# Optimization experiments

Measured on AMD Instinct MI355X. Metric: run time of the kernel, lower is better.

Reference implementation:

```python
import jax, jax.numpy as jnp
import numpy as np

N_USER, N_MOVIE, H, E = 100000, 50000, 512, 500000

def setup_inputs() -> dict:
    key = jax.random.key(0)
    ks = jax.random.split(key, 8)
    z_user = jax.random.normal(ks[0], (N_USER, H), dtype=jnp.float32)
    z_movie = jax.random.normal(ks[1], (N_MOVIE, H), dtype=jnp.float32)
    edge_row = jax.random.randint(ks[2], (E,), 0, N_USER, dtype=jnp.int64)
    edge_col = jax.random.randint(ks[3], (E,), 0, N_MOVIE, dtype=jnp.int64)
    w1 = jax.random.normal(ks[4], (2 * H, H), dtype=jnp.float32) * (1.0 / np.sqrt(2 * H))
    b1 = jax.random.normal(ks[5], (H,), dtype=jnp.float32) * 0.01
    w2 = jax.random.normal(ks[6], (H, 1), dtype=jnp.float32) * (1.0 / np.sqrt(H))
    b2 = jax.random.normal(ks[7], (1,), dtype=jnp.float32) * 0.01
    return {"z_user": z_user, "z_movie": z_movie, "edge_row": edge_row,
            "edge_col": edge_col, "w1": w1, "b1": b1, "w2": w2, "b2": b2}

def reference(z_user, z_movie, edge_row, edge_col, w1, b1, w2, b2):
    # Gather endpoint embeddings and concat -> [E, 2H]
    z = jnp.concatenate([z_user[edge_row], z_movie[edge_col]], axis=-1)
    h = jax.nn.relu(z @ w1 + b1)      # [E, H]
    out = h @ w2 + b2                 # [E, 1]
    return out.reshape(-1)
```

## Files before the change

kernel.cpp:

```cpp
#include <hip/hip_runtime.h>
#include <hip/hip_bf16.h>

typedef __attribute__((ext_vector_type(8))) short bf16x8;
typedef __attribute__((ext_vector_type(4))) float f32x4;

#define HDIM 512
#define BM 128
#define BN 256
#define BK 64
#define BKP 72

__device__ __forceinline__ unsigned short f2bf(float f) {
  unsigned u = __float_as_uint(f);
  u += 0x7fffu + ((u >> 16) & 1u);
  return (unsigned short)(u >> 16);
}

__device__ __forceinline__ unsigned int pk_bf(float x, float y) {
  __hip_bfloat162 h = __float22bfloat162_rn(float2{x, y});
  union { __hip_bfloat162 b; unsigned int u; } cv; cv.b = h;
  return cv.u;
}

__global__ void k_w1t(const float* __restrict__ w1, unsigned short* __restrict__ w1t,
                      int* __restrict__ cnt, int nzero) {
  int idx = blockIdx.x * 256 + threadIdx.x;
  int k = idx >> 9;
  int n = idx & 511;
  w1t[n * 1024 + k] = f2bf(w1[idx]);
  if (idx < nzero) cnt[idx] = 0;
}

__global__ void k_hist(const int* __restrict__ ec, int* __restrict__ cnt, int E) {
  int e = blockIdx.x * 256 + threadIdx.x;
  if (e < E) atomicAdd(&cnt[ec[e]], 1);
}

__global__ __launch_bounds__(1024) void k_scan(const int* __restrict__ cnt, int* __restrict__ ptr,
                                               int* __restrict__ cur, int n) {
  __shared__ int wsum[16];
  __shared__ int carry_s;
  const int tid = threadIdx.x, lane = tid & 63, w = tid >> 6;
  if (tid == 0) carry_s = 0;
  __syncthreads();
  for (int base = 0; base < n; base += 1024) {
    int i = base + tid;
    int x = (i < n) ? cnt[i] : 0;
    int v = x;
    #pragma unroll
    for (int off = 1; off < 64; off <<= 1) {
      int t = __shfl_up(v, off, 64);
      if (lane >= off) v += t;
    }
    if (lane == 63) wsum[w] = v;
    __syncthreads();
    int wpre = 0;
    #pragma unroll
    for (int j = 0; j < 16; ++j) { int s = wsum[j]; if (j < w) wpre += s; }
    int carry = carry_s;
    __syncthreads();
    int incl = v + wpre;
    if (i < n) { int excl = carry + incl - x; ptr[i] = excl; cur[i] = excl; }
    if (tid == 1023) carry_s = carry + incl;
    __syncthreads();
  }
  if (threadIdx.x == 0) ptr[n] = carry_s;
}

__global__ void k_scatter(const int* __restrict__ er, const int* __restrict__ ec,
                          int* __restrict__ cur, int* __restrict__ srow,
                          int* __restrict__ seid, int E) {
  int e = blockIdx.x * 256 + threadIdx.x;
  if (e < E) {
    int c = ec[e];
    int pos = atomicAdd(&cur[c], 1);
    srow[pos] = er[e];
    seid[pos] = e;
  }
}

__global__ __launch_bounds__(512) void k_gemm(const float* __restrict__ A, int M,
    const unsigned short* __restrict__ w1t, int koff,
    unsigned short* __restrict__ C)
{
  __shared__ unsigned short As[BM][BKP];
  __shared__ unsigned short Bs[BN][BKP];
  const int tid  = threadIdx.x;
  const int lane = tid & 63;
  const int wid  = tid >> 6;
  const int wm = wid & 1, wn = wid >> 1;
  const int lm = lane & 15, lq = lane >> 4;
  const int nbase = blockIdx.x * BN;
  const int mbase = blockIdx.y * BM;

  f32x4 acc[4][4];
  #pragma unroll
  for (int i = 0; i < 4; ++i)
    #pragma unroll
    for (int j = 0; j < 4; ++j) acc[i][j] = (f32x4){0.f, 0.f, 0.f, 0.f};

  for (int kb = 0; kb < HDIM / BK; ++kb) {
    const int k0 = kb * BK;
    __syncthreads();
    #pragma unroll
    for (int i = 0; i < 4; ++i) {
      int fid = i * 512 + tid;
      int r = fid >> 4, c4 = fid & 15;
      int row = mbase + r; if (row > M - 1) row = M - 1;
      const float4 v = *(const float4*)&A[(size_t)row * HDIM + k0 + c4 * 4];
      unsigned int* dst = (unsigned int*)&As[r][c4 * 4];
      dst[0] = pk_bf(v.x, v.y);
      dst[1] = pk_bf(v.z, v.w);
    }
    #pragma unroll
    for (int i = 0; i < 4; ++i) {
      int cid = i * 512 + tid;
      int r = cid >> 3, c8 = cid & 7;
      const bf16x8 g = *(const bf16x8*)&w1t[(size_t)(nbase + r) * 1024 + koff + k0 + c8 * 8];
      *(bf16x8*)&Bs[r][c8 * 8] = g;
    }
    __syncthreads();
    #pragma unroll
    for (int ks = 0; ks < 2; ++ks) {
      bf16x8 af[4], bfr[4];
      #pragma unroll
      for (int t = 0; t < 4; ++t) {
        af[t]  = *(const bf16x8*)&As[wm * 64 + t * 16 + lm][ks * 32 + lq * 8];
        bfr[t] = *(const bf16x8*)&Bs[wn * 64 + t * 16 + lm][ks * 32 + lq * 8];
      }
      #pragma unroll
      for (int mi = 0; mi < 4; ++mi)
        #pragma unroll
        for (int ni = 0; ni < 4; ++ni)
          acc[mi][ni] = __builtin_amdgcn_mfma_f32_16x16x32_bf16(af[mi], bfr[ni], acc[mi][ni], 0, 0, 0);
    }
  }
  #pragma unroll
  for (int mi = 0; mi < 4; ++mi)
    #pragma unroll
    for (int ni = 0; ni < 4; ++ni)
      #pragma unroll
      for (int r = 0; r < 4; ++r) {
        int rg = mbase + wm * 64 + mi * 16 + lq * 4 + r;
        int cg = nbase + wn * 64 + ni * 16 + lm;
        if (rg < M) C[(size_t)rg * HDIM + cg] = f2bf(acc[mi][ni][r]);
      }
}

__device__ __forceinline__ float edot(const uint4 ua, const float* vb, const float* wv) {
  float p = 0.f, s;
  s = __uint_as_float(ua.x << 16)         + vb[0]; s = fmaxf(s, 0.f); p += s * wv[0];
  s = __uint_as_float(ua.x & 0xffff0000u) + vb[1]; s = fmaxf(s, 0.f); p += s * wv[1];
  s = __uint_as_float(ua.y << 16)         + vb[2]; s = fmaxf(s, 0.f); p += s * wv[2];
  s = __uint_as_float(ua.y & 0xffff0000u) + vb[3]; s = fmaxf(s, 0.f); p += s * wv[3];
  s = __uint_as_float(ua.z << 16)         + vb[4]; s = fmaxf(s, 0.f); p += s * wv[4];
  s = __uint_as_float(ua.z & 0xffff0000u) + vb[5]; s = fmaxf(s, 0.f); p += s * wv[5];
  s = __uint_as_float(ua.w << 16)         + vb[6]; s = fmaxf(s, 0.f); p += s * wv[6];
  s = __uint_as_float(ua.w & 0xffff0000u) + vb[7]; s = fmaxf(s, 0.f); p += s * wv[7];
  return p;
}

__global__ __launch_bounds__(256) void k_edge_g(const int* __restrict__ ptr,
    const int* __restrict__ srow, const int* __restrict__ seid,
    const unsigned short* __restrict__ u1, const unsigned short* __restrict__ m1,
    const float* __restrict__ b1, const float* __restrict__ w2, const float* __restrict__ b2,
    float* __restrict__ out, int nmov)
{
  const int lane = threadIdx.x & 63;
  const int gw = blockIdx.x * 4 + (threadIdx.x >> 6);
  const int nw = gridDim.x * 4;
  const float4 b1a = *(const float4*)&b1[lane * 8];
  const float4 b1b = *(const float4*)&b1[lane * 8 + 4];
  const float4 w2a = *(const float4*)&w2[lane * 8];
  const float4 w2b = *(const float4*)&w2[lane * 8 + 4];
  float wv[8] = {w2a.x, w2a.y, w2a.z, w2a.w, w2b.x, w2b.y, w2b.z, w2b.w};
  const float bias2 = b2[0];
  for (int c = gw; c < nmov; c += nw) {
    const int beg = ptr[c], end = ptr[c + 1];
    if (beg == end) continue;
    const uint4 va = *(const uint4*)&m1[(size_t)c * HDIM + lane * 8];
    float vb[8];
    vb[0] = __uint_as_float(va.x << 16)         + b1a.x;
    vb[1] = __uint_as_float(va.x & 0xffff0000u) + b1a.y;
    vb[2] = __uint_as_float(va.y << 16)         + b1a.z;
    vb[3] = __uint_as_float(va.y & 0xffff0000u) + b1a.w;
    vb[4] = __uint_as_float(va.z << 16)         + b1b.x;
    vb[5] = __uint_as_float(va.z & 0xffff0000u) + b1b.y;
    vb[6] = __uint_as_float(va.w << 16)         + b1b.z;
    vb[7] = __uint_as_float(va.w & 0xffff0000u) + b1b.w;
    int i = beg;
    for (; i + 1 < end; i += 2) {
      const int r0 = srow[i], r1 = srow[i + 1];
      const int e0 = seid[i], e1 = seid[i + 1];
      const uint4 ua0 = *(const uint4*)&u1[(size_t)r0 * HDIM + lane * 8];
      const uint4 ua1 = *(const uint4*)&u1[(size_t)r1 * HDIM + lane * 8];
      float p0 = edot(ua0, vb, wv);
      float p1 = edot(ua1, vb, wv);
      #pragma unroll
      for (int off = 32; off > 0; off >>= 1) {
        p0 += __shfl_down(p0, off, 64);
        p1 += __shfl_down(p1, off, 64);
      }
      if (lane == 0) { out[e0] = p0 + bias2; out[e1] = p1 + bias2; }
    }
    if (i < end) {
      const int r0 = srow[i], e0 = seid[i];
      const uint4 ua0 = *(const uint4*)&u1[(size_t)r0 * HDIM + lane * 8];
      float p0 = edot(ua0, vb, wv);
      #pragma unroll
      for (int off = 32; off > 0; off >>= 1) p0 += __shfl_down(p0, off, 64);
      if (lane == 0) out[e0] = p0 + bias2;
    }
  }
}

__global__ __launch_bounds__(256) void k_edge(const int* __restrict__ er, const int* __restrict__ ec,
    const unsigned short* __restrict__ u1, const unsigned short* __restrict__ m1,
    const float* __restrict__ b1, const float* __restrict__ w2, const float* __restrict__ b2,
    float* __restrict__ out, int E)
{
  const int lane = threadIdx.x & 63;
  const int gwid = blockIdx.x * 4 + (threadIdx.x >> 6);
  const int nw   = gridDim.x * 4;
  const float4 b1a = *(const float4*)&b1[lane * 8];
  const float4 b1b = *(const float4*)&b1[lane * 8 + 4];
  const float4 w2a = *(const float4*)&w2[lane * 8];
  const float4 w2b = *(const float4*)&w2[lane * 8 + 4];
  float bv[8] = {b1a.x, b1a.y, b1a.z, b1a.w, b1b.x, b1b.y, b1b.z, b1b.w};
  float wv[8] = {w2a.x, w2a.y, w2a.z, w2a.w, w2b.x, w2b.y, w2b.z, w2b.w};
  const float bias2 = b2[0];
  for (int e = gwid; e < E; e += nw) {
    const int r = er[e], c = ec[e];
    const uint4 ua = *(const uint4*)&u1[(size_t)r * HDIM + lane * 8];
    const uint4 va = *(const uint4*)&m1[(size_t)c * HDIM + lane * 8];
    float vb[8];
    vb[0] = __uint_as_float(va.x << 16)         + bv[0];
    vb[1] = __uint_as_float(va.x & 0xffff0000u) + bv[1];
    vb[2] = __uint_as_float(va.y << 16)         + bv[2];
    vb[3] = __uint_as_float(va.y & 0xffff0000u) + bv[3];
    vb[4] = __uint_as_float(va.z << 16)         + bv[4];
    vb[5] = __uint_as_float(va.z & 0xffff0000u) + bv[5];
    vb[6] = __uint_as_float(va.w << 16)         + bv[6];
    vb[7] = __uint_as_float(va.w & 0xffff0000u) + bv[7];
    float p = edot(ua, vb, wv);
    #pragma unroll
    for (int off = 32; off > 0; off >>= 1) p += __shfl_down(p, off, 64);
    if (lane == 0) out[e] = p + bias2;
  }
}

__global__ __launch_bounds__(256) void k_fallback(const float* __restrict__ zu, const float* __restrict__ zm,
    const int* __restrict__ er, const int* __restrict__ ec, const float* __restrict__ w1,
    const float* __restrict__ b1, const float* __restrict__ w2, const float* __restrict__ b2,
    float* __restrict__ out, int E)
{
  __shared__ float Zs[64][33];
  __shared__ float Ws[32][65];
  __shared__ float outacc[64];
  __shared__ int ridx[64], cidx[64];
  const int tid = threadIdx.x;
  const int ebase = blockIdx.x * 64;
  if (tid < 64) {
    int e = ebase + tid; if (e > E - 1) e = E - 1;
    ridx[tid] = er[e]; cidx[tid] = ec[e];
    outacc[tid] = 0.f;
  }
  const int tx = tid & 15, ty = tid >> 4;
  for (int nt = 0; nt < 8; ++nt) {
    float acc[4][4] = {};
    for (int kc = 0; kc < 32; ++kc) {
      __syncthreads();
      #pragma unroll
      for (int i = 0; i < 8; ++i) {
        int id = i * 256 + tid;
        int rr = id >> 5, cc = id & 31;
        int k = kc * 32 + cc;
        Zs[rr][cc] = (k < 512) ? zu[(size_t)ridx[rr] * 512 + k]
                               : zm[(size_t)cidx[rr] * 512 + (k - 512)];
      }
      #pragma unroll
      for (int i = 0; i < 8; ++i) {
        int id = i * 256 + tid;
        int kk = id >> 6, nn = id & 63;
        Ws[kk][nn] = w1[(size_t)(kc * 32 + kk) * 512 + nt * 64 + nn];
      }
      __syncthreads();
      #pragma unroll
      for (int kk = 0; kk < 32; ++kk) {
        float a0 = Zs[ty*4+0][kk], a1 = Zs[ty*4+1][kk], a2 = Zs[ty*4+2][kk], a3 = Zs[ty*4+3][kk];
        float q0 = Ws[kk][tx*4+0], q1 = Ws[kk][tx*4+1], q2 = Ws[kk][tx*4+2], q3 = Ws[kk][tx*4+3];
        acc[0][0] += a0*q0; acc[0][1] += a0*q1; acc[0][2] += a0*q2; acc[0][3] += a0*q3;
        acc[1][0] += a1*q0; acc[1][1] += a1*q1; acc[1][2] += a1*q2; acc[1][3] += a1*q3;
        acc[2][0] += a2*q0; acc[2][1] += a2*q1; acc[2][2] += a2*q2; acc[2][3] += a2*q3;
        acc[3][0] += a3*q0; acc[3][1] += a3*q1; acc[3][2] += a3*q2; acc[3][3] += a3*q3;
      }
    }
    #pragma unroll
    for (int i = 0; i < 4; ++i) {
      float p = 0.f;
      #pragma unroll
      for (int j = 0; j < 4; ++j) {
        int n = nt * 64 + tx * 4 + j;
        float h = acc[i][j] + b1[n]; h = fmaxf(h, 0.f);
        p += h * w2[n];
      }
      atomicAdd(&outacc[ty * 4 + i], p);
    }
  }
  __syncthreads();
  if (tid < 64 && (ebase + tid) < E) out[ebase + tid] = outacc[tid] + b2[0];
}

extern "C" void kernel_launch(void* const* d_in, const int* in_sizes, int n_in,
                              void* d_out, int out_size, void* d_ws, size_t ws_size,
                              hipStream_t stream)
{
  const float* z_user  = (const float*)d_in[0];
  const float* z_movie = (const float*)d_in[1];
  const int*   erow    = (const int*)d_in[2];
  const int*   ecol    = (const int*)d_in[3];
  const float* w1      = (const float*)d_in[4];
  const float* b1      = (const float*)d_in[5];
  const float* w2      = (const float*)d_in[6];
  const float* b2      = (const float*)d_in[7];
  float* out = (float*)d_out;

  const int NU = in_sizes[0] / HDIM;
  const int NM = in_sizes[1] / HDIM;
  const int E  = in_sizes[2];

  const size_t shorts = (size_t)(NU + NM) * HDIM + (size_t)1024 * 512;
  const size_t need_basic  = shorts * 2;
  const size_t need_sorted = shorts * 2 + ((size_t)3 * NM + 1 + (size_t)2 * E) * 4;

  if (ws_size >= need_basic) {
    unsigned short* u1  = (unsigned short*)d_ws;
    unsigned short* m1  = u1 + (size_t)NU * HDIM;
    unsigned short* w1t = m1 + (size_t)NM * HDIM;
    if (ws_size >= need_sorted) {
      int* cnt  = (int*)(w1t + (size_t)1024 * 512);
      int* ptr  = cnt + NM;
      int* cur  = ptr + NM + 1;
      int* srow = cur + NM;
      int* seid = srow + E;
      k_w1t<<<(1024 * 512) / 256, 256, 0, stream>>>(w1, w1t, cnt, NM);
      k_hist<<<(E + 255) / 256, 256, 0, stream>>>(ecol, cnt, E);
      k_scan<<<1, 1024, 0, stream>>>(cnt, ptr, cur, NM);
      k_scatter<<<(E + 255) / 256, 256, 0, stream>>>(erow, ecol, cur, srow, seid, E);
      k_gemm<<<dim3(HDIM / BN, (NU + BM - 1) / BM), 512, 0, stream>>>(z_user,  NU, w1t, 0,   u1);
      k_gemm<<<dim3(HDIM / BN, (NM + BM - 1) / BM), 512, 0, stream>>>(z_movie, NM, w1t, 512, m1);
      k_edge_g<<<2048, 256, 0, stream>>>(ptr, srow, seid, u1, m1, b1, w2, b2, out, NM);
    } else {
      k_w1t<<<(1024 * 512) / 256, 256, 0, stream>>>(w1, w1t, (int*)d_ws, 0);
      k_gemm<<<dim3(HDIM / BN, (NU + BM - 1) / BM), 512, 0, stream>>>(z_user,  NU, w1t, 0,   u1);
      k_gemm<<<dim3(HDIM / BN, (NM + BM - 1) / BM), 512, 0, stream>>>(z_movie, NM, w1t, 512, m1);
      k_edge<<<2048, 256, 0, stream>>>(erow, ecol, u1, m1, b1, w2, b2, out, E);
    }
  } else {
    k_fallback<<<(E + 63) / 64, 256, 0, stream>>>(z_user, z_movie, erow, ecol, w1, b1, w2, b2, out, E);
  }
}
```

Baseline: 643.2 us.

## Use direct global-to-LDS loads with XOR swizzle in GEMM and parallelize scan

```diff
diff --git a/kernel.cpp b/kernel.cpp
--- a/kernel.cpp
+++ b/kernel.cpp
@@ -8,7 +8,6 @@
 #define BM 128
 #define BN 256
 #define BK 64
-#define BKP 72
 
 __device__ __forceinline__ unsigned short f2bf(float f) {
   unsigned u = __float_as_uint(f);
@@ -20,6 +19,12 @@
   __hip_bfloat162 h = __float22bfloat162_rn(float2{x, y});
   union { __hip_bfloat162 b; unsigned int u; } cv; cv.b = h;
   return cv.u;
+}
+
+__device__ __forceinline__ void glds16(const void* g, void* l) {
+  __builtin_amdgcn_global_load_lds(
+      (const __attribute__((address_space(1))) void*)g,
+      (__attribute__((address_space(3))) void*)l, 16, 0, 0);
 }
 
 __global__ void k_w1t(const float* __restrict__ w1, unsigned short* __restrict__ w1t,
@@ -36,35 +41,64 @@
   if (e < E) atomicAdd(&cnt[ec[e]], 1);
 }
 
-__global__ __launch_bounds__(1024) void k_scan(const int* __restrict__ cnt, int* __restrict__ ptr,
-                                               int* __restrict__ cur, int n) {
-  __shared__ int wsum[16];
-  __shared__ int carry_s;
+__global__ __launch_bounds__(1024) void k_scan1(const int* __restrict__ cnt,
+                                                int* __restrict__ bsum, int n) {
+  __shared__ int ws[16];
   const int tid = threadIdx.x, lane = tid & 63, w = tid >> 6;
-  if (tid == 0) carry_s = 0;
+  int i = blockIdx.x * 1024 + tid;
+  int x = (i < n) ? cnt[i] : 0;
+  #pragma unroll
+  for (int off = 32; off > 0; off >>= 1) x += __shfl_down(x, off, 64);
+  if (lane == 0) ws[w] = x;
   __syncthreads();
-  for (int base = 0; base < n; base += 1024) {
-    int i = base + tid;
-    int x = (i < n) ? cnt[i] : 0;
-    int v = x;
-    #pragma unroll
-    for (int off = 1; off < 64; off <<= 1) {
-      int t = __shfl_up(v, off, 64);
-      if (lane >= off) v += t;
-    }
-    if (lane == 63) wsum[w] = v;
-    __syncthreads();
-    int wpre = 0;
-    #pragma unroll
-    for (int j = 0; j < 16; ++j) { int s = wsum[j]; if (j < w) wpre += s; }
-    int carry = carry_s;
-    __syncthreads();
-    int incl = v + wpre;
-    if (i < n) { int excl = carry + incl - x; ptr[i] = excl; cur[i] = excl; }
-    if (tid == 1023) carry_s = carry + incl;
-    __syncthreads();
-  }
-  if (threadIdx.x == 0) ptr[n] = carry_s;
+  if (tid == 0) {
+    int s = 0;
+    #pragma unroll
+    for (int j = 0; j < 16; ++j) s += ws[j];
+    bsum[blockIdx.x] = s;
+  }
+}
+
+__global__ void k_scan2(int* __restrict__ bsum, int* __restrict__ ptr, int nb, int n) {
+  const int tid = threadIdx.x;
+  if (nb > 64) {
+    if (tid == 0) {
+      int s = 0;
+      for (int j = 0; j < nb; ++j) { int v = bsum[j]; bsum[j] = s; s += v; }
+      ptr[n] = s;
+    }
+    return;
+  }
+  int x = (tid < nb) ? bsum[tid] : 0;
+  int v = x;
+  #pragma unroll
+  for (int off = 1; off < 64; off <<= 1) {
+    int t = __shfl_up(v, off, 64);
+    if (tid >= off) v += t;
+  }
+  if (tid < nb) bsum[tid] = v - x;
+  if (tid == 63) ptr[n] = v;
+}
+
+__global__ __launch_bounds__(1024) void k_scan3(const int* __restrict__ cnt,
+    const int* __restrict__ bsum, int* __restrict__ ptr, int* __restrict__ cur, int n) {
+  __shared__ int ws[16];
+  const int tid = threadIdx.x, lane = tid & 63, w = tid >> 6;
+  int i = blockIdx.x * 1024 + tid;
+  int x = (i < n) ? cnt[i] : 0;
+  int v = x;
+  #pragma unroll
+  for (int off = 1; off < 64; off <<= 1) {
+    int t = __shfl_up(v, off, 64);
+    if (lane >= off) v += t;
+  }
+  if (lane == 63) ws[w] = v;
+  __syncthreads();
+  int wpre = 0;
+  #pragma unroll
+  for (int j = 0; j < 16; ++j) { int s = ws[j]; if (j < w) wpre += s; }
+  int excl = bsum[blockIdx.x] + wpre + v - x;
+  if (i < n) { ptr[i] = excl; cur[i] = excl; }
 }
 
 __global__ void k_scatter(const int* __restrict__ er, const int* __restrict__ ec,
@@ -79,15 +113,16 @@
   }
 }
 
-__global__ __launch_bounds__(512) void k_gemm(const float* __restrict__ A, int M,
+__global__ __launch_bounds__(512, 4) void k_gemm(const float* __restrict__ A, int M,
     const unsigned short* __restrict__ w1t, int koff,
     unsigned short* __restrict__ C)
 {
-  __shared__ unsigned short As[BM][BKP];
-  __shared__ unsigned short Bs[BN][BKP];
+  __shared__ float          As[BM * BK];
+  __shared__ unsigned short Bs[BN * BK];
   const int tid  = threadIdx.x;
   const int lane = tid & 63;
   const int wid  = tid >> 6;
+  const int wuni = wid << 6;
   const int wm = wid & 1, wn = wid >> 1;
   const int lm = lane & 15, lq = lane >> 4;
   const int nbase = blockIdx.x * BN;
@@ -104,35 +139,48 @@
     __syncthreads();
     #pragma unroll
     for (int i = 0; i < 4; ++i) {
-      int fid = i * 512 + tid;
-      int r = fid >> 4, c4 = fid & 15;
+      int G  = i * 512 + tid;
+      int Gw = i * 512 + wuni;
+      int r = G >> 4, gr = G & 15;
       int row = mbase + r; if (row > M - 1) row = M - 1;
-      const float4 v = *(const float4*)&A[(size_t)row * HDIM + k0 + c4 * 4];
-      unsigned int* dst = (unsigned int*)&As[r][c4 * 4];
-      dst[0] = pk_bf(v.x, v.y);
-      dst[1] = pk_bf(v.z, v.w);
+      int cg = gr ^ (r & 15);
+      glds16(&A[(size_t)row * HDIM + k0 + cg * 4], (char*)As + (size_t)Gw * 16);
     }
     #pragma unroll
     for (int i = 0; i < 4; ++i) {
-      int cid = i * 512 + tid;
-      int r = cid >> 3, c8 = cid & 7;
-      const bf16x8 g = *(const bf16x8*)&w1t[(size_t)(nbase + r) * 1024 + koff + k0 + c8 * 8];
-      *(bf16x8*)&Bs[r][c8 * 8] = g;
+      int G  = i * 512 + tid;
+      int Gw = i * 512 + wuni;
+      int r = G >> 3, gr = G & 7;
+      int cg = gr ^ (r & 7);
+      glds16(&w1t[(size_t)(nbase + r) * 1024 + koff + k0 + cg * 8],
+             (char*)Bs + (size_t)Gw * 16);
     }
     __syncthreads();
     #pragma unroll
     for (int ks = 0; ks < 2; ++ks) {
-      bf16x8 af[4], bfr[4];
-      #pragma unroll
-      for (int t = 0; t < 4; ++t) {
-        af[t]  = *(const bf16x8*)&As[wm * 64 + t * 16 + lm][ks * 32 + lq * 8];
-        bfr[t] = *(const bf16x8*)&Bs[wn * 64 + t * 16 + lm][ks * 32 + lq * 8];
-      }
-      #pragma unroll
-      for (int mi = 0; mi < 4; ++mi)
+      bf16x8 bfr[4];
+      #pragma unroll
+      for (int ni = 0; ni < 4; ++ni) {
+        int R = wn * 64 + ni * 16 + lm;
+        int g = (ks * 4 + lq) ^ (R & 7);
+        bfr[ni] = *(const bf16x8*)&Bs[(size_t)(R * 8 + g) * 8];
+      }
+      #pragma unroll
+      for (int mi = 0; mi < 4; ++mi) {
+        int R = wm * 64 + mi * 16 + lm;
+        int g0 = ks * 8 + lq * 2;
+        int m  = R & 15;
+        const float4 f0 = *(const float4*)&As[(size_t)(R * 16 + (g0 ^ m)) * 4];
+        const float4 f1 = *(const float4*)&As[(size_t)(R * 16 + ((g0 + 1) ^ m)) * 4];
+        union { unsigned int u[4]; bf16x8 v; } af;
+        af.u[0] = pk_bf(f0.x, f0.y);
+        af.u[1] = pk_bf(f0.z, f0.w);
+        af.u[2] = pk_bf(f1.x, f1.y);
+        af.u[3] = pk_bf(f1.z, f1.w);
         #pragma unroll
         for (int ni = 0; ni < 4; ++ni)
-          acc[mi][ni] = __builtin_amdgcn_mfma_f32_16x16x32_bf16(af[mi], bfr[ni], acc[mi][ni], 0, 0, 0);
+          acc[mi][ni] = __builtin_amdgcn_mfma_f32_16x16x32_bf16(af.v, bfr[ni], acc[mi][ni], 0, 0, 0);
+      }
     }
   }
   #pragma unroll
@@ -328,10 +376,11 @@
   const int NU = in_sizes[0] / HDIM;
   const int NM = in_sizes[1] / HDIM;
   const int E  = in_sizes[2];
+  const int NB = (NM + 1023) / 1024;
 
   const size_t shorts = (size_t)(NU + NM) * HDIM + (size_t)1024 * 512;
   const size_t need_basic  = shorts * 2;
-  const size_t need_sorted = shorts * 2 + ((size_t)3 * NM + 1 + (size_t)2 * E) * 4;
+  const size_t need_sorted = shorts * 2 + ((size_t)3 * NM + 1 + (size_t)2 * E + NB + 64) * 4;
 
   if (ws_size >= need_basic) {
     unsigned short* u1  = (unsigned short*)d_ws;
@@ -343,9 +392,12 @@
       int* cur  = ptr + NM + 1;
       int* srow = cur + NM;
       int* seid = srow + E;
+      int* bsum = seid + E;
       k_w1t<<<(1024 * 512) / 256, 256, 0, stream>>>(w1, w1t, cnt, NM);
       k_hist<<<(E + 255) / 256, 256, 0, stream>>>(ecol, cnt, E);
-      k_scan<<<1, 1024, 0, stream>>>(cnt, ptr, cur, NM);
+      k_scan1<<<NB, 1024, 0, stream>>>(cnt, bsum, NM);
+      k_scan2<<<1, 64, 0, stream>>>(bsum, ptr, NB, NM);
+      k_scan3<<<NB, 1024, 0, stream>>>(cnt, bsum, ptr, cur, NM);
       k_scatter<<<(E + 255) / 256, 256, 0, stream>>>(erow, ecol, cur, srow, seid, E);
       k_gemm<<<dim3(HDIM / BN, (NU + BM - 1) / BM), 512, 0, stream>>>(z_user,  NU, w1t, 0,   u1);
       k_gemm<<<dim3(HDIM / BN, (NM + BM - 1) / BM), 512, 0, stream>>>(z_movie, NM, w1t, 512, m1);
```

New measurement: 602.2 us. -6.4%, faster.
